# Optimization experiments

Hardware: AMD Instinct MI355X
Metric: run time of the kernel (lower is better)

Reference implementation:

```python
import jax, jax.numpy as jnp
import numpy as np

N = 50000        # num_nodes
E = 800000       # num_edges
D_IN = 128
D_OUT = 128
BN_EPS = 1e-5    # torch BatchNorm1d default


def setup_inputs() -> dict:
    key = jax.random.key(0)
    ks = jax.random.split(key, 6)
    x = jax.random.normal(ks[0], (N, D_IN), dtype=jnp.float32)
    edge_index = jax.random.randint(ks[1], (2, E), 0, N, dtype=jnp.int64)
    eps = jnp.zeros((1,), dtype=jnp.float32)  # nn.Parameter(torch.tensor([0.0]))
    lim1 = 1.0 / np.sqrt(D_IN)
    lim2 = 1.0 / np.sqrt(D_OUT)
    W1 = jax.random.uniform(ks[2], (D_OUT, D_IN), jnp.float32, -lim1, lim1)
    b1 = jax.random.uniform(ks[3], (D_OUT,), jnp.float32, -lim1, lim1)
    W2 = jax.random.uniform(ks[4], (D_OUT, D_OUT), jnp.float32, -lim2, lim2)
    b2 = jax.random.uniform(ks[5], (D_OUT,), jnp.float32, -lim2, lim2)
    gamma1 = jnp.ones((D_OUT,), jnp.float32)
    beta1 = jnp.zeros((D_OUT,), jnp.float32)
    gamma2 = jnp.ones((D_OUT,), jnp.float32)
    beta2 = jnp.zeros((D_OUT,), jnp.float32)
    return {"x": x, "edge_index": edge_index, "eps": eps,
            "W1": W1, "b1": b1, "gamma1": gamma1, "beta1": beta1,
            "W2": W2, "b2": b2, "gamma2": gamma2, "beta2": beta2}


def _batch_norm(h, gamma, beta):
    # training-mode BatchNorm1d: biased batch variance, eps=1e-5
    mu = h.mean(axis=0)
    var = h.var(axis=0)
    return gamma * (h - mu) * jax.lax.rsqrt(var + BN_EPS) + beta


def reference(x, edge_index, eps, W1, b1, gamma1, beta1, W2, b2, gamma2, beta2):
    row, col = edge_index[0], edge_index[1]
    # agg[v] = sum_{(v,u) in edges} x[u]   (gather + scatter-add)
    agg = jax.ops.segment_sum(x[col], row, num_segments=N)  # [N, D_IN]
    out = (1.0 + eps) * x + agg                              # [N, D_IN]
    h = jax.nn.relu(_batch_norm(out @ W1.T + b1, gamma1, beta1))
    h = jax.nn.relu(_batch_norm(h @ W2.T + b2, gamma2, beta2))
    return h
```

## Files before the change

kernel.cpp:

```cpp
#include <hip/hip_runtime.h>

#define NN 50000
#define EE 800000
#define DD 128
#define BN_EPS 1e-5f
#define XCONV_B 3125
#define BIN_BLOCKS 200
#define BIN_EDGES 4000
#define NBUCK 3125
#define BROWS 16
#define BCAP 512
#define NREP 32
#define GEMM_B 782
#define LDA 136
#define ZROW NN

typedef __attribute__((ext_vector_type(8))) short bf16x8;
typedef __attribute__((ext_vector_type(4))) float f32x4;
typedef __attribute__((ext_vector_type(8))) unsigned short u16x8;

__device__ inline unsigned short f2bf(float f) {
  unsigned int u = __float_as_uint(f);
  u = (u + 0x7fffu + ((u >> 16) & 1u)) >> 16;
  return (unsigned short)u;
}
__device__ inline float bf2f(unsigned short b) {
  return __uint_as_float(((unsigned int)b) << 16);
}
__device__ inline int colof(const unsigned short* sc, int i, int e) {
  const unsigned short v = sc[i < e ? i : 0];
  return i < e ? (int)v : ZROW;
}


__global__ __launch_bounds__(256) void k_prep(const float* __restrict__ x,
                                              const float* __restrict__ W1,
                                              const float* __restrict__ W2,
                                              unsigned short* __restrict__ xb,
                                              unsigned short* __restrict__ W1b,
                                              unsigned short* __restrict__ W2b,
                                              int* __restrict__ bcur,
                                              float* __restrict__ reps) {
  const int b = blockIdx.x;
  const int t = threadIdx.x;
  if (b < XCONV_B) {
    const int gid = b * 256 + t;
    const float4 v0 = ((const float4*)x)[gid * 2];
    const float4 v1 = ((const float4*)x)[gid * 2 + 1];
    ushort4 o0, o1;
    o0.x = f2bf(v0.x); o0.y = f2bf(v0.y); o0.z = f2bf(v0.z); o0.w = f2bf(v0.w);
    o1.x = f2bf(v1.x); o1.y = f2bf(v1.y); o1.z = f2bf(v1.z); o1.w = f2bf(v1.w);
    ((ushort4*)xb)[gid * 2] = o0;
    ((ushort4*)xb)[gid * 2 + 1] = o1;
    if (gid <= NBUCK) bcur[gid] = 0;
    if (gid < 4 * NREP * DD) reps[gid] = 0.0f;
    if (gid < 16) {
      const ushort4 z = {0, 0, 0, 0};
      ((ushort4*)(xb + (size_t)NN * DD))[gid * 2] = z;
      ((ushort4*)(xb + (size_t)NN * DD))[gid * 2 + 1] = z;
    }
  } else if (b < XCONV_B + 16) {
    const int gid = (b - XCONV_B) * 256 + t;
    const float4 v = ((const float4*)W1)[gid];
    ushort4 o;
    o.x = f2bf(v.x); o.y = f2bf(v.y); o.z = f2bf(v.z); o.w = f2bf(v.w);
    ((ushort4*)W1b)[gid] = o;
  } else {
    const int gid = (b - XCONV_B - 16) * 256 + t;
    const float4 v = ((const float4*)W2)[gid];
    ushort4 o;
    o.x = f2bf(v.x); o.y = f2bf(v.y); o.z = f2bf(v.z); o.w = f2bf(v.w);
    ((ushort4*)W2b)[gid] = o;
  }
}

__global__ __launch_bounds__(256) void k_bin0(const int* __restrict__ rows,
                                              const int* __restrict__ cols,
                                              int* __restrict__ bcur,
                                              unsigned int* __restrict__ bbuf) {
  __shared__ int hist[NBUCK];
  __shared__ int lbase[NBUCK];
  const int t = threadIdx.x;
  for (int i = t; i < NBUCK; i += 256) hist[i] = 0;
  __syncthreads();
  const int e0 = blockIdx.x * BIN_EDGES;
  int er[16], ec[16];
#pragma unroll
  for (int i = 0; i < 16; ++i) {
    const int idx = t + i * 256;
    if (idx < BIN_EDGES) {
      er[i] = rows[e0 + idx];
      ec[i] = cols[e0 + idx];
      atomicAdd(&hist[er[i] >> 4], 1);
    }
  }
  __syncthreads();
  for (int i = t; i < NBUCK; i += 256) {
    const int c = hist[i];
    lbase[i] = (c > 0) ? atomicAdd(&bcur[i], c) : 0;
    hist[i] = 0;
  }
  __syncthreads();
#pragma unroll
  for (int i = 0; i < 16; ++i) {
    const int idx = t + i * 256;
    if (idx < BIN_EDGES) {
      const int bk = er[i] >> 4;
      const int lp = lbase[bk] + atomicAdd(&hist[bk], 1);
      if (lp < BCAP)
        bbuf[(size_t)bk * BCAP + lp] =
            ((unsigned)(er[i] & 15) << 16) | (unsigned)ec[i];
    }
  }
}

#define ISSUE(P, Q, I0, I1)                                            \
  P##0 = *(const u16x8*)(xb + (size_t)colof(scols, (I0), end0) * DD + l16 * 8); \
  P##1 = *(const u16x8*)(xb + (size_t)colof(scols, (I0) + 4, end0) * DD + l16 * 8); \
  P##2 = *(const u16x8*)(xb + (size_t)colof(scols, (I0) + 8, end0) * DD + l16 * 8); \
  P##3 = *(const u16x8*)(xb + (size_t)colof(scols, (I0) + 12, end0) * DD + l16 * 8); \
  Q##0 = *(const u16x8*)(xb + (size_t)colof(scols, (I1), end1) * DD + l16 * 8); \
  Q##1 = *(const u16x8*)(xb + (size_t)colof(scols, (I1) + 4, end1) * DD + l16 * 8); \
  Q##2 = *(const u16x8*)(xb + (size_t)colof(scols, (I1) + 8, end1) * DD + l16 * 8); \
  Q##3 = *(const u16x8*)(xb + (size_t)colof(scols, (I1) + 12, end1) * DD + l16 * 8);

#define CONSUME(P, Q)                                                  \
  _Pragma("unroll") for (int j = 0; j < 8; ++j) {                      \
    a0[j] += (bf2f(P##0[j]) + bf2f(P##1[j])) +                         \
             (bf2f(P##2[j]) + bf2f(P##3[j]));                          \
    a1[j] += (bf2f(Q##0[j]) + bf2f(Q##1[j])) +                         \
             (bf2f(Q##2[j]) + bf2f(Q##3[j]));                          \
  }

__global__ __launch_bounds__(128) void k_aggemm1(
    const unsigned short* __restrict__ xb, const float* __restrict__ eps,
    const int* __restrict__ bcnt, const unsigned int* __restrict__ bbuf,
    const unsigned short* __restrict__ W, const float* __restrict__ bias,
    unsigned short* __restrict__ outb, float* __restrict__ sum1r,
    float* __restrict__ sumsq1r) {
  __shared__ unsigned short scols[BCAP];
  __shared__ unsigned short sA[BROWS * LDA];
  __shared__ int rcnt[BROWS];
  __shared__ int roff[BROWS + 1];
  const int t = threadIdx.x;
  const int bk = blockIdx.x;
  const int wv = t >> 6;
  const int lane = t & 63;
  const int sub = lane >> 4;
  const int l16 = lane & 15;

  int n = bcnt[bk];
  n = n < BCAP ? n : BCAP;
  if (t < BROWS) rcnt[t] = 0;
  __syncthreads();

  unsigned int ent[4];
  int nl = 0;
  for (int i = t; i < n; i += 128) {
    const unsigned int e = bbuf[(size_t)bk * BCAP + i];
    ent[nl++] = e;
    atomicAdd(&rcnt[e >> 16], 1);
  }
  __syncthreads();
  if (t < BROWS) {
    int v = rcnt[t];
#pragma unroll
    for (int off = 1; off < BROWS; off <<= 1) {
      const int u = __shfl_up(v, off);
      if (lane >= off) v += u;
    }
    roff[t] = v - rcnt[t];
    if (t == BROWS - 1) roff[BROWS] = v;
    rcnt[t] = 0;
  }
  __syncthreads();
  for (int i = 0; i < nl; ++i) {
    const int r = ent[i] >> 16;
    const int pos = roff[r] + atomicAdd(&rcnt[r], 1);
    scols[pos] = (unsigned short)(ent[i] & 0xffffu);
  }
  __syncthreads();

  {
    const float s = 1.0f + eps[0];
#pragma unroll
    for (int rr = 0; rr < 4; ++rr) {
      const int r0 = wv + rr * 4;
      const int r1 = r0 + 2;
      float a0[8], a1[8];
#pragma unroll
      for (int j = 0; j < 8; ++j) { a0[j] = 0.f; a1[j] = 0.f; }
      if (sub < 2) {
        const int selfrow = bk * BROWS + (sub == 0 ? r0 : r1);
        const u16x8 a = *(const u16x8*)(xb + (size_t)selfrow * DD + l16 * 8);
        if (sub == 0) {
#pragma unroll
          for (int j = 0; j < 8; ++j) a0[j] = s * bf2f(a[j]);
        } else {
#pragma unroll
          for (int j = 0; j < 8; ++j) a1[j] = s * bf2f(a[j]);
        }
      }
      const int end0 = roff[r0 + 1];
      const int end1 = roff[r1 + 1];
      const int n0 = end0 - roff[r0];
      const int n1 = end1 - roff[r1];
      int i0 = roff[r0] + sub;
      int i1 = roff[r1] + sub;
      int nb = (n0 > n1 ? n0 : n1);
      nb = (nb + 15) >> 4;
      u16x8 pa0, pa1, pa2, pa3, qa0, qa1, qa2, qa3;
      u16x8 pb0, pb1, pb2, pb3, qb0, qb1, qb2, qb3;
      if (nb > 0) {
        ISSUE(pa, qa, i0, i1);
        i0 += 16; i1 += 16;
        int k = nb - 1;
        while (k >= 2) {
          ISSUE(pb, qb, i0, i1);
          i0 += 16; i1 += 16;
          CONSUME(pa, qa);
          ISSUE(pa, qa, i0, i1);
          i0 += 16; i1 += 16;
          CONSUME(pb, qb);
          k -= 2;
        }
        if (k == 1) {
          ISSUE(pb, qb, i0, i1);
          CONSUME(pa, qa);
          CONSUME(pb, qb);
        } else {
          CONSUME(pa, qa);
        }
      }
#pragma unroll
      for (int j = 0; j < 8; ++j) {
        a0[j] += __shfl_xor(a0[j], 16);
        a0[j] += __shfl_xor(a0[j], 32);
        a1[j] += __shfl_xor(a1[j], 16);
        a1[j] += __shfl_xor(a1[j], 32);
      }
      if (sub < 2) {
        u16x8 o;
        if (sub == 0) {
#pragma unroll
          for (int j = 0; j < 8; ++j) o[j] = f2bf(a0[j]);
          *(u16x8*)(&sA[r0 * LDA + l16 * 8]) = o;
        } else {
#pragma unroll
          for (int j = 0; j < 8; ++j) o[j] = f2bf(a1[j]);
          *(u16x8*)(&sA[r1 * LDA + l16 * 8]) = o;
        }
      }
    }
  }
  __syncthreads();

  f32x4 acc[4];
#pragma unroll
  for (int nn = 0; nn < 4; ++nn) acc[nn] = (f32x4){0.f, 0.f, 0.f, 0.f};
#pragma unroll
  for (int kk = 0; kk < 4; ++kk) {
    const bf16x8 af = *(const bf16x8*)(&sA[l16 * LDA + kk * 32 + sub * 8]);
#pragma unroll
    for (int nn = 0; nn < 4; ++nn) {
      const bf16x8 bf = *(const bf16x8*)(
          W + (size_t)(wv * 64 + nn * 16 + l16) * DD + sub * 8 + kk * 32);
      acc[nn] = __builtin_amdgcn_mfma_f32_16x16x32_bf16(af, bf, acc[nn], 0, 0, 0);
    }
  }
  const int orow0 = bk * BROWS + sub * 4;
  const int rep = (bk & (NREP - 1)) * DD;
#pragma unroll
  for (int nn = 0; nn < 4; ++nn) {
    const int col = wv * 64 + nn * 16 + l16;
    const float bv = bias[col];
    float sv = 0.f, qv = 0.f;
#pragma unroll
    for (int r = 0; r < 4; ++r) {
      const float o = acc[nn][r] + bv;
      outb[(size_t)(orow0 + r) * DD + col] = f2bf(o);
      sv += o; qv += o * o;
    }
    sv += __shfl_xor(sv, 16); qv += __shfl_xor(qv, 16);
    sv += __shfl_xor(sv, 32); qv += __shfl_xor(qv, 32);
    if (sub == 0) {
      atomicAdd(&sum1r[rep + col], sv);
      atomicAdd(&sumsq1r[rep + col], qv);
    }
  }
}

__global__ __launch_bounds__(256) void k_gemm2(const unsigned short* __restrict__ A,
                                               const float* __restrict__ sum1r,
                                               const float* __restrict__ sumsq1r,
                                               const float* __restrict__ gamma,
                                               const float* __restrict__ beta,
                                               const unsigned short* __restrict__ W,
                                               const float* __restrict__ bias,
                                               unsigned short* __restrict__ outb,
                                               float* __restrict__ sum2r,
                                               float* __restrict__ sumsq2r,
                                               const float* __restrict__ gamma2,
                                               const float* __restrict__ beta2,
                                               float* __restrict__ scale2,
                                               float* __restrict__ shift2,
                                               int* __restrict__ done) {
  __shared__ float lsc[DD];
  __shared__ float lsh[DD];
  __shared__ float bsum[DD];
  __shared__ float bsq[DD];
  __shared__ int amlast;
  const int tid = threadIdx.x;
  const int wv = tid >> 6;
  const int lane = tid & 63;
  const int quad = lane >> 4;
  const int l16 = lane & 15;
  if (tid < DD) {
    float sm = 0.f, qm = 0.f;
#pragma unroll
    for (int r = 0; r < NREP; ++r) {
      sm += sum1r[r * DD + tid];
      qm += sumsq1r[r * DD + tid];
    }
    const float inv_n = 1.0f / (float)NN;
    const float mean = sm * inv_n;
    const float var = qm * inv_n - mean * mean;
    const float s = gamma[tid] * rsqrtf(var + BN_EPS);
    lsc[tid] = s;
    lsh[tid] = beta[tid] - mean * s;
    bsum[tid] = 0.f;
    bsq[tid] = 0.f;
  }
  __syncthreads();

  const int rowbase = blockIdx.x * 64 + wv * 16 + l16;
  const int arow = rowbase < NN ? rowbase : NN - 1;
  const unsigned short* aptr = A + (size_t)arow * DD + quad * 8;

  f32x4 acc[8];
#pragma unroll
  for (int n = 0; n < 8; ++n) acc[n] = (f32x4){0.f, 0.f, 0.f, 0.f};
#pragma unroll
  for (int kk = 0; kk < 4; ++kk) {
    const int kbase = kk * 32 + quad * 8;
    const u16x8 a = *(const u16x8*)(aptr + kk * 32);
    const float4 s0 = *(const float4*)&lsc[kbase];
    const float4 s1 = *(const float4*)&lsc[kbase + 4];
    const float4 h0 = *(const float4*)&lsh[kbase];
    const float4 h1 = *(const float4*)&lsh[kbase + 4];
    bf16x8 af;
    af[0] = (short)f2bf(fmaxf(fmaf(s0.x, bf2f(a[0]), h0.x), 0.f));
    af[1] = (short)f2bf(fmaxf(fmaf(s0.y, bf2f(a[1]), h0.y), 0.f));
    af[2] = (short)f2bf(fmaxf(fmaf(s0.z, bf2f(a[2]), h0.z), 0.f));
    af[3] = (short)f2bf(fmaxf(fmaf(s0.w, bf2f(a[3]), h0.w), 0.f));
    af[4] = (short)f2bf(fmaxf(fmaf(s1.x, bf2f(a[4]), h1.x), 0.f));
    af[5] = (short)f2bf(fmaxf(fmaf(s1.y, bf2f(a[5]), h1.y), 0.f));
    af[6] = (short)f2bf(fmaxf(fmaf(s1.z, bf2f(a[6]), h1.z), 0.f));
    af[7] = (short)f2bf(fmaxf(fmaf(s1.w, bf2f(a[7]), h1.w), 0.f));
#pragma unroll
    for (int n = 0; n < 8; ++n) {
      const bf16x8 bf =
          *(const bf16x8*)(W + (size_t)(n * 16 + l16) * DD + kbase);
      acc[n] = __builtin_amdgcn_mfma_f32_16x16x32_bf16(af, bf, acc[n], 0, 0, 0);
    }
  }
  const int orow0 = blockIdx.x * 64 + wv * 16 + quad * 4;
#pragma unroll
  for (int n = 0; n < 8; ++n) {
    const int col = n * 16 + l16;
    const float bv = bias[col];
    float sv = 0.f, qv = 0.f;
#pragma unroll
    for (int r = 0; r < 4; ++r) {
      const int row = orow0 + r;
      if (row < NN) {
        const float o = acc[n][r] + bv;
        outb[(size_t)row * DD + col] = f2bf(o);
        sv += o; qv += o * o;
      }
    }
    sv += __shfl_xor(sv, 16); qv += __shfl_xor(qv, 16);
    sv += __shfl_xor(sv, 32); qv += __shfl_xor(qv, 32);
    if (quad == 0) { atomicAdd(&bsum[col], sv); atomicAdd(&bsq[col], qv); }
  }
  __syncthreads();
  if (tid < DD) {
    const int rep = (blockIdx.x & (NREP - 1)) * DD;
    atomicAdd(&sum2r[rep + tid], bsum[tid]);
    atomicAdd(&sumsq2r[rep + tid], bsq[tid]);
  }
  __syncthreads();
  if (tid == 0) amlast = (atomicAdd(done, 1) == GEMM_B - 1) ? 1 : 0;
  __syncthreads();
  if (amlast) {
    if (tid < DD) {
      float sm = 0.f, qm = 0.f;
#pragma unroll
      for (int r = 0; r < NREP; ++r) {
        sm += __hip_atomic_load(&sum2r[r * DD + tid], __ATOMIC_RELAXED,
                                __HIP_MEMORY_SCOPE_AGENT);
        qm += __hip_atomic_load(&sumsq2r[r * DD + tid], __ATOMIC_RELAXED,
                                __HIP_MEMORY_SCOPE_AGENT);
      }
      const float inv_n = 1.0f / (float)NN;
      const float mean = sm * inv_n;
      const float var = qm * inv_n - mean * mean;
      const float sc = gamma2[tid] * rsqrtf(var + BN_EPS);
      scale2[tid] = sc;
      shift2[tid] = beta2[tid] - mean * sc;
    }
  }
}

__global__ __launch_bounds__(256) void k_bnrelu(const unsigned short* __restrict__ in,
                                                const float* __restrict__ scale,
                                                const float* __restrict__ shift,
                                                float* __restrict__ out) {
  __shared__ float lsc[DD];
  __shared__ float lsh[DD];
  const int t = threadIdx.x;
  if (t < DD) {
    lsc[t] = scale[t];
    lsh[t] = shift[t];
  }
  __syncthreads();
  const int gid = blockIdx.x * 256 + t;
  const int c = (gid & 15) * 8;
  const u16x8 a = ((const u16x8*)in)[gid];
  const float4 sc0 = *(const float4*)&lsc[c];
  const float4 sc1 = *(const float4*)&lsc[c + 4];
  const float4 sh0 = *(const float4*)&lsh[c];
  const float4 sh1 = *(const float4*)&lsh[c + 4];
  float4 o0, o1;
  o0.x = fmaxf(fmaf(sc0.x, bf2f(a[0]), sh0.x), 0.f);
  o0.y = fmaxf(fmaf(sc0.y, bf2f(a[1]), sh0.y), 0.f);
  o0.z = fmaxf(fmaf(sc0.z, bf2f(a[2]), sh0.z), 0.f);
  o0.w = fmaxf(fmaf(sc0.w, bf2f(a[3]), sh0.w), 0.f);
  o1.x = fmaxf(fmaf(sc1.x, bf2f(a[4]), sh1.x), 0.f);
  o1.y = fmaxf(fmaf(sc1.y, bf2f(a[5]), sh1.y), 0.f);
  o1.z = fmaxf(fmaf(sc1.z, bf2f(a[6]), sh1.z), 0.f);
  o1.w = fmaxf(fmaf(sc1.w, bf2f(a[7]), sh1.w), 0.f);
  ((float4*)out)[gid * 2] = o0;
  ((float4*)out)[gid * 2 + 1] = o1;
}

extern "C" void kernel_launch(void* const* d_in, const int* in_sizes, int n_in,
                              void* d_out, int out_size, void* d_ws, size_t ws_size,
                              hipStream_t stream) {
  const float* x = (const float*)d_in[0];
  const int* ei = (const int*)d_in[1];
  const float* eps = (const float*)d_in[2];
  const float* W1 = (const float*)d_in[3];
  const float* b1 = (const float*)d_in[4];
  const float* g1 = (const float*)d_in[5];
  const float* be1 = (const float*)d_in[6];
  const float* W2 = (const float*)d_in[7];
  const float* b2 = (const float*)d_in[8];
  const float* g2 = (const float*)d_in[9];
  const float* be2 = (const float*)d_in[10];
  float* out = (float*)d_out;

  const int* rows = ei;
  const int* cols = ei + EE;

  int* bcur = (int*)d_out;
  unsigned short* xb = (unsigned short*)d_out + 2000000;
  unsigned int* bbuf = (unsigned int*)((char*)d_out + 16800256);
  unsigned short* W1b = (unsigned short*)d_out + 11640000;
  unsigned short* W2b = (unsigned short*)d_out + 11680000;
  float* reps = (float*)d_out + 5875000;
  float* sum1r = reps;
  float* sumsq1r = reps + NREP * DD;
  float* sum2r = reps + 2 * NREP * DD;
  float* sumsq2r = reps + 3 * NREP * DD;
  int* done = bcur + NBUCK;

  unsigned short* h1b = (unsigned short*)d_ws;
  unsigned short* h2b = h1b + (size_t)NN * DD;
  float* stats = (float*)(h1b + (size_t)2 * NN * DD);
  float* scale2 = stats + 0;
  float* shift2 = stats + 128;

  k_prep<<<XCONV_B + 32, 256, 0, stream>>>(x, W1, W2, xb, W1b, W2b, bcur, reps);
  k_bin0<<<BIN_BLOCKS, 256, 0, stream>>>(rows, cols, bcur, bbuf);
  k_aggemm1<<<NBUCK, 128, 0, stream>>>(xb, eps, bcur, bbuf, W1b, b1, h1b,
                                       sum1r, sumsq1r);
  k_gemm2<<<GEMM_B, 256, 0, stream>>>(h1b, sum1r, sumsq1r, g1, be1, W2b, b2,
                                      h2b, sum2r, sumsq2r, g2, be2,
                                      scale2, shift2, done);
  k_bnrelu<<<(NN * DD / 8) / 256, 256, 0, stream>>>(h2b, scale2, shift2, out);
}
```

Before: 209.0 us.

## Merge prep and binning kernels, skip idle gathers, double rows per gemm2 wave

The x/W bf16 conversion and the edge-binning pass now run in one launch, with extra blocks doing the binning, and the bucket counter reset moves to a hipMemsetAsync. In the aggregation kernel each of the two rows in a pair now issues and consumes its gathers only while it still has edges left, so short rows no longer load the zero row. The second GEMM has each wave compute 32 rows with two MFMA accumulator sets, halving the block count and reusing each W fragment twice. The costs are more registers in gemm2, fewer blocks to spread across CUs, and an added memset in place of the in-kernel reset.

```diff
diff --git a/kernel.cpp b/kernel.cpp
--- a/kernel.cpp
+++ b/kernel.cpp
@@ -11,7 +11,7 @@
 #define BROWS 16
 #define BCAP 512
 #define NREP 32
-#define GEMM_B 782
+#define GEMM2B 391
 #define LDA 136
 #define ZROW NN
 
@@ -33,14 +33,15 @@
 }
 
 
-__global__ __launch_bounds__(256) void k_prep(const float* __restrict__ x,
-                                              const float* __restrict__ W1,
-                                              const float* __restrict__ W2,
-                                              unsigned short* __restrict__ xb,
-                                              unsigned short* __restrict__ W1b,
-                                              unsigned short* __restrict__ W2b,
-                                              int* __restrict__ bcur,
-                                              float* __restrict__ reps) {
+__global__ __launch_bounds__(256) void k_prepbin(
+    const float* __restrict__ x, const float* __restrict__ W1,
+    const float* __restrict__ W2, const int* __restrict__ rows,
+    const int* __restrict__ cols, unsigned short* __restrict__ xb,
+    unsigned short* __restrict__ W1b, unsigned short* __restrict__ W2b,
+    int* __restrict__ bcur, unsigned int* __restrict__ bbuf,
+    float* __restrict__ reps) {
+  __shared__ int hist[NBUCK];
+  __shared__ int lbase[NBUCK];
   const int b = blockIdx.x;
   const int t = threadIdx.x;
   if (b < XCONV_B) {
@@ -52,7 +53,6 @@
     o1.x = f2bf(v1.x); o1.y = f2bf(v1.y); o1.z = f2bf(v1.z); o1.w = f2bf(v1.w);
     ((ushort4*)xb)[gid * 2] = o0;
     ((ushort4*)xb)[gid * 2 + 1] = o1;
-    if (gid <= NBUCK) bcur[gid] = 0;
     if (gid < 4 * NREP * DD) reps[gid] = 0.0f;
     if (gid < 16) {
       const ushort4 z = {0, 0, 0, 0};
@@ -65,72 +65,66 @@
     ushort4 o;
     o.x = f2bf(v.x); o.y = f2bf(v.y); o.z = f2bf(v.z); o.w = f2bf(v.w);
     ((ushort4*)W1b)[gid] = o;
-  } else {
+  } else if (b < XCONV_B + 32) {
     const int gid = (b - XCONV_B - 16) * 256 + t;
     const float4 v = ((const float4*)W2)[gid];
     ushort4 o;
     o.x = f2bf(v.x); o.y = f2bf(v.y); o.z = f2bf(v.z); o.w = f2bf(v.w);
     ((ushort4*)W2b)[gid] = o;
-  }
-}
-
-__global__ __launch_bounds__(256) void k_bin0(const int* __restrict__ rows,
-                                              const int* __restrict__ cols,
-                                              int* __restrict__ bcur,
-                                              unsigned int* __restrict__ bbuf) {
-  __shared__ int hist[NBUCK];
-  __shared__ int lbase[NBUCK];
-  const int t = threadIdx.x;
-  for (int i = t; i < NBUCK; i += 256) hist[i] = 0;
-  __syncthreads();
-  const int e0 = blockIdx.x * BIN_EDGES;
-  int er[16], ec[16];
-#pragma unroll
-  for (int i = 0; i < 16; ++i) {
-    const int idx = t + i * 256;
-    if (idx < BIN_EDGES) {
-      er[i] = rows[e0 + idx];
-      ec[i] = cols[e0 + idx];
-      atomicAdd(&hist[er[i] >> 4], 1);
-    }
-  }
-  __syncthreads();
-  for (int i = t; i < NBUCK; i += 256) {
-    const int c = hist[i];
-    lbase[i] = (c > 0) ? atomicAdd(&bcur[i], c) : 0;
-    hist[i] = 0;
-  }
-  __syncthreads();
-#pragma unroll
-  for (int i = 0; i < 16; ++i) {
-    const int idx = t + i * 256;
-    if (idx < BIN_EDGES) {
-      const int bk = er[i] >> 4;
-      const int lp = lbase[bk] + atomicAdd(&hist[bk], 1);
-      if (lp < BCAP)
-        bbuf[(size_t)bk * BCAP + lp] =
-            ((unsigned)(er[i] & 15) << 16) | (unsigned)ec[i];
-    }
-  }
-}
-
-#define ISSUE(P, Q, I0, I1)                                            \
-  P##0 = *(const u16x8*)(xb + (size_t)colof(scols, (I0), end0) * DD + l16 * 8); \
-  P##1 = *(const u16x8*)(xb + (size_t)colof(scols, (I0) + 4, end0) * DD + l16 * 8); \
-  P##2 = *(const u16x8*)(xb + (size_t)colof(scols, (I0) + 8, end0) * DD + l16 * 8); \
-  P##3 = *(const u16x8*)(xb + (size_t)colof(scols, (I0) + 12, end0) * DD + l16 * 8); \
-  Q##0 = *(const u16x8*)(xb + (size_t)colof(scols, (I1), end1) * DD + l16 * 8); \
-  Q##1 = *(const u16x8*)(xb + (size_t)colof(scols, (I1) + 4, end1) * DD + l16 * 8); \
-  Q##2 = *(const u16x8*)(xb + (size_t)colof(scols, (I1) + 8, end1) * DD + l16 * 8); \
-  Q##3 = *(const u16x8*)(xb + (size_t)colof(scols, (I1) + 12, end1) * DD + l16 * 8);
-
-#define CONSUME(P, Q)                                                  \
-  _Pragma("unroll") for (int j = 0; j < 8; ++j) {                      \
-    a0[j] += (bf2f(P##0[j]) + bf2f(P##1[j])) +                         \
-             (bf2f(P##2[j]) + bf2f(P##3[j]));                          \
-    a1[j] += (bf2f(Q##0[j]) + bf2f(Q##1[j])) +                         \
-             (bf2f(Q##2[j]) + bf2f(Q##3[j]));                          \
-  }
+  } else {
+    const int bb = b - XCONV_B - 32;
+    for (int i = t; i < NBUCK; i += 256) hist[i] = 0;
+    __syncthreads();
+    const int e0 = bb * BIN_EDGES;
+    int er[16], ec[16];
+#pragma unroll
+    for (int i = 0; i < 16; ++i) {
+      const int idx = t + i * 256;
+      if (idx < BIN_EDGES) {
+        er[i] = rows[e0 + idx];
+        ec[i] = cols[e0 + idx];
+        atomicAdd(&hist[er[i] >> 4], 1);
+      }
+    }
+    __syncthreads();
+    for (int i = t; i < NBUCK; i += 256) {
+      const int c = hist[i];
+      lbase[i] = (c > 0) ? atomicAdd(&bcur[i], c) : 0;
+      hist[i] = 0;
+    }
+    __syncthreads();
+#pragma unroll
+    for (int i = 0; i < 16; ++i) {
+      const int idx = t + i * 256;
+      if (idx < BIN_EDGES) {
+        const int bk = er[i] >> 4;
+        const int lp = lbase[bk] + atomicAdd(&hist[bk], 1);
+        if (lp < BCAP)
+          bbuf[(size_t)bk * BCAP + lp] =
+              ((unsigned)(er[i] & 15) << 16) | (unsigned)ec[i];
+      }
+    }
+  }
+}
+
+#define ISSUE_P(P, I)                                                  \
+  P##0 = *(const u16x8*)(xb + (size_t)colof(scols, (I), end0) * DD + l16 * 8); \
+  P##1 = *(const u16x8*)(xb + (size_t)colof(scols, (I) + 4, end0) * DD + l16 * 8); \
+  P##2 = *(const u16x8*)(xb + (size_t)colof(scols, (I) + 8, end0) * DD + l16 * 8); \
+  P##3 = *(const u16x8*)(xb + (size_t)colof(scols, (I) + 12, end0) * DD + l16 * 8);
+#define ISSUE_Q(Q, I)                                                  \
+  Q##0 = *(const u16x8*)(xb + (size_t)colof(scols, (I), end1) * DD + l16 * 8); \
+  Q##1 = *(const u16x8*)(xb + (size_t)colof(scols, (I) + 4, end1) * DD + l16 * 8); \
+  Q##2 = *(const u16x8*)(xb + (size_t)colof(scols, (I) + 8, end1) * DD + l16 * 8); \
+  Q##3 = *(const u16x8*)(xb + (size_t)colof(scols, (I) + 12, end1) * DD + l16 * 8);
+#define CONS_P(P)                                                      \
+  _Pragma("unroll") for (int j = 0; j < 8; ++j)                        \
+      a0[j] += (bf2f(P##0[j]) + bf2f(P##1[j])) +                       \
+               (bf2f(P##2[j]) + bf2f(P##3[j]));
+#define CONS_Q(Q)                                                      \
+  _Pragma("unroll") for (int j = 0; j < 8; ++j)                        \
+      a1[j] += (bf2f(Q##0[j]) + bf2f(Q##1[j])) +                       \
+               (bf2f(Q##2[j]) + bf2f(Q##3[j]));
 
 __global__ __launch_bounds__(128) void k_aggemm1(
     const unsigned short* __restrict__ xb, const float* __restrict__ eps,
@@ -212,24 +206,35 @@
       u16x8 pa0, pa1, pa2, pa3, qa0, qa1, qa2, qa3;
       u16x8 pb0, pb1, pb2, pb3, qb0, qb1, qb2, qb3;
       if (nb > 0) {
-        ISSUE(pa, qa, i0, i1);
-        i0 += 16; i1 += 16;
+        int off = 0, aoff = 0, boff = 0;
+        if (off < n0) { ISSUE_P(pa, i0); }
+        if (off < n1) { ISSUE_Q(qa, i1); }
+        aoff = off; off += 16; i0 += 16; i1 += 16;
         int k = nb - 1;
         while (k >= 2) {
-          ISSUE(pb, qb, i0, i1);
-          i0 += 16; i1 += 16;
-          CONSUME(pa, qa);
-          ISSUE(pa, qa, i0, i1);
-          i0 += 16; i1 += 16;
-          CONSUME(pb, qb);
+          if (off < n0) { ISSUE_P(pb, i0); }
+          if (off < n1) { ISSUE_Q(qb, i1); }
+          boff = off; off += 16; i0 += 16; i1 += 16;
+          if (aoff < n0) { CONS_P(pa); }
+          if (aoff < n1) { CONS_Q(qa); }
+          if (off < n0) { ISSUE_P(pa, i0); }
+          if (off < n1) { ISSUE_Q(qa, i1); }
+          aoff = off; off += 16; i0 += 16; i1 += 16;
+          if (boff < n0) { CONS_P(pb); }
+          if (boff < n1) { CONS_Q(qb); }
           k -= 2;
         }
         if (k == 1) {
-          ISSUE(pb, qb, i0, i1);
-          CONSUME(pa, qa);
-          CONSUME(pb, qb);
+          if (off < n0) { ISSUE_P(pb, i0); }
+          if (off < n1) { ISSUE_Q(qb, i1); }
+          boff = off;
+          if (aoff < n0) { CONS_P(pa); }
+          if (aoff < n1) { CONS_Q(qa); }
+          if (boff < n0) { CONS_P(pb); }
+          if (boff < n1) { CONS_Q(qb); }
         } else {
-          CONSUME(pa, qa);
+          if (aoff < n0) { CONS_P(pa); }
+          if (aoff < n1) { CONS_Q(qa); }
         }
       }
 #pragma unroll
@@ -333,52 +338,68 @@
   }
   __syncthreads();
 
-  const int rowbase = blockIdx.x * 64 + wv * 16 + l16;
-  const int arow = rowbase < NN ? rowbase : NN - 1;
-  const unsigned short* aptr = A + (size_t)arow * DD + quad * 8;
-
-  f32x4 acc[8];
-#pragma unroll
-  for (int n = 0; n < 8; ++n) acc[n] = (f32x4){0.f, 0.f, 0.f, 0.f};
+  const int rb0 = blockIdx.x * 128 + wv * 32 + l16;
+  const int ar0 = rb0 < NN ? rb0 : NN - 1;
+  const int ar1 = (rb0 + 16) < NN ? (rb0 + 16) : NN - 1;
+  const unsigned short* ap0 = A + (size_t)ar0 * DD + quad * 8;
+  const unsigned short* ap1 = A + (size_t)ar1 * DD + quad * 8;
+
+  f32x4 acc[2][8];
+#pragma unroll
+  for (int m = 0; m < 2; ++m)
+#pragma unroll
+    for (int n = 0; n < 8; ++n) acc[m][n] = (f32x4){0.f, 0.f, 0.f, 0.f};
 #pragma unroll
   for (int kk = 0; kk < 4; ++kk) {
     const int kbase = kk * 32 + quad * 8;
-    const u16x8 a = *(const u16x8*)(aptr + kk * 32);
+    const u16x8 x0 = *(const u16x8*)(ap0 + kk * 32);
+    const u16x8 x1 = *(const u16x8*)(ap1 + kk * 32);
     const float4 s0 = *(const float4*)&lsc[kbase];
     const float4 s1 = *(const float4*)&lsc[kbase + 4];
     const float4 h0 = *(const float4*)&lsh[kbase];
     const float4 h1 = *(const float4*)&lsh[kbase + 4];
-    bf16x8 af;
-    af[0] = (short)f2bf(fmaxf(fmaf(s0.x, bf2f(a[0]), h0.x), 0.f));
-    af[1] = (short)f2bf(fmaxf(fmaf(s0.y, bf2f(a[1]), h0.y), 0.f));
-    af[2] = (short)f2bf(fmaxf(fmaf(s0.z, bf2f(a[2]), h0.z), 0.f));
-    af[3] = (short)f2bf(fmaxf(fmaf(s0.w, bf2f(a[3]), h0.w), 0.f));
-    af[4] = (short)f2bf(fmaxf(fmaf(s1.x, bf2f(a[4]), h1.x), 0.f));
-    af[5] = (short)f2bf(fmaxf(fmaf(s1.y, bf2f(a[5]), h1.y), 0.f));
-    af[6] = (short)f2bf(fmaxf(fmaf(s1.z, bf2f(a[6]), h1.z), 0.f));
-    af[7] = (short)f2bf(fmaxf(fmaf(s1.w, bf2f(a[7]), h1.w), 0.f));
+    bf16x8 af0, af1;
+    af0[0] = (short)f2bf(fmaxf(fmaf(s0.x, bf2f(x0[0]), h0.x), 0.f));
+    af0[1] = (short)f2bf(fmaxf(fmaf(s0.y, bf2f(x0[1]), h0.y), 0.f));
+    af0[2] = (short)f2bf(fmaxf(fmaf(s0.z, bf2f(x0[2]), h0.z), 0.f));
+    af0[3] = (short)f2bf(fmaxf(fmaf(s0.w, bf2f(x0[3]), h0.w), 0.f));
+    af0[4] = (short)f2bf(fmaxf(fmaf(s1.x, bf2f(x0[4]), h1.x), 0.f));
+    af0[5] = (short)f2bf(fmaxf(fmaf(s1.y, bf2f(x0[5]), h1.y), 0.f));
+    af0[6] = (short)f2bf(fmaxf(fmaf(s1.z, bf2f(x0[6]), h1.z), 0.f));
+    af0[7] = (short)f2bf(fmaxf(fmaf(s1.w, bf2f(x0[7]), h1.w), 0.f));
+    af1[0] = (short)f2bf(fmaxf(fmaf(s0.x, bf2f(x1[0]), h0.x), 0.f));
+    af1[1] = (short)f2bf(fmaxf(fmaf(s0.y, bf2f(x1[1]), h0.y), 0.f));
+    af1[2] = (short)f2bf(fmaxf(fmaf(s0.z, bf2f(x1[2]), h0.z), 0.f));
+    af1[3] = (short)f2bf(fmaxf(fmaf(s0.w, bf2f(x1[3]), h0.w), 0.f));
+    af1[4] = (short)f2bf(fmaxf(fmaf(s1.x, bf2f(x1[4]), h1.x), 0.f));
+    af1[5] = (short)f2bf(fmaxf(fmaf(s1.y, bf2f(x1[5]), h1.y), 0.f));
+    af1[6] = (short)f2bf(fmaxf(fmaf(s1.z, bf2f(x1[6]), h1.z), 0.f));
+    af1[7] = (short)f2bf(fmaxf(fmaf(s1.w, bf2f(x1[7]), h1.w), 0.f));
 #pragma unroll
     for (int n = 0; n < 8; ++n) {
       const bf16x8 bf =
           *(const bf16x8*)(W + (size_t)(n * 16 + l16) * DD + kbase);
-      acc[n] = __builtin_amdgcn_mfma_f32_16x16x32_bf16(af, bf, acc[n], 0, 0, 0);
-    }
-  }
-  const int orow0 = blockIdx.x * 64 + wv * 16 + quad * 4;
+      acc[0][n] = __builtin_amdgcn_mfma_f32_16x16x32_bf16(af0, bf, acc[0][n], 0, 0, 0);
+      acc[1][n] = __builtin_amdgcn_mfma_f32_16x16x32_bf16(af1, bf, acc[1][n], 0, 0, 0);
+    }
+  }
+  const int orow0 = blockIdx.x * 128 + wv * 32 + quad * 4;
 #pragma unroll
   for (int n = 0; n < 8; ++n) {
     const int col = n * 16 + l16;
     const float bv = bias[col];
     float sv = 0.f, qv = 0.f;
 #pragma unroll
-    for (int r = 0; r < 4; ++r) {
-      const int row = orow0 + r;
-      if (row < NN) {
-        const float o = acc[n][r] + bv;
-        outb[(size_t)row * DD + col] = f2bf(o);
-        sv += o; qv += o * o;
-      }
-    }
+    for (int m = 0; m < 2; ++m)
+#pragma unroll
+      for (int r = 0; r < 4; ++r) {
+        const int row = orow0 + m * 16 + r;
+        if (row < NN) {
+          const float o = acc[m][n][r] + bv;
+          outb[(size_t)row * DD + col] = f2bf(o);
+          sv += o; qv += o * o;
+        }
+      }
     sv += __shfl_xor(sv, 16); qv += __shfl_xor(qv, 16);
     sv += __shfl_xor(sv, 32); qv += __shfl_xor(qv, 32);
     if (quad == 0) { atomicAdd(&bsum[col], sv); atomicAdd(&bsq[col], qv); }
@@ -390,7 +411,7 @@
     atomicAdd(&sumsq2r[rep + tid], bsq[tid]);
   }
   __syncthreads();
-  if (tid == 0) amlast = (atomicAdd(done, 1) == GEMM_B - 1) ? 1 : 0;
+  if (tid == 0) amlast = (atomicAdd(done, 1) == GEMM2B - 1) ? 1 : 0;
   __syncthreads();
   if (amlast) {
     if (tid < DD) {
@@ -481,11 +502,12 @@
   float* scale2 = stats + 0;
   float* shift2 = stats + 128;
 
-  k_prep<<<XCONV_B + 32, 256, 0, stream>>>(x, W1, W2, xb, W1b, W2b, bcur, reps);
-  k_bin0<<<BIN_BLOCKS, 256, 0, stream>>>(rows, cols, bcur, bbuf);
+  hipMemsetAsync(bcur, 0, (NBUCK + 1) * sizeof(int), stream);
+  k_prepbin<<<XCONV_B + 32 + BIN_BLOCKS, 256, 0, stream>>>(
+      x, W1, W2, rows, cols, xb, W1b, W2b, bcur, bbuf, reps);
   k_aggemm1<<<NBUCK, 128, 0, stream>>>(xb, eps, bcur, bbuf, W1b, b1, h1b,
                                        sum1r, sumsq1r);
-  k_gemm2<<<GEMM_B, 256, 0, stream>>>(h1b, sum1r, sumsq1r, g1, be1, W2b, b2,
+  k_gemm2<<<GEMM2B, 256, 0, stream>>>(h1b, sum1r, sumsq1r, g1, be1, W2b, b2,
                                       h2b, sum2r, sumsq2r, g2, be2,
                                       scale2, shift2, done);
   k_bnrelu<<<(NN * DD / 8) / 256, 256, 0, stream>>>(h2b, scale2, shift2, out);
```

After: 212.7 us. About the same (+1.8%).
